# Performance work log

Measured on AMD Instinct MI355X. Metric: run time of the kernel, lower is better.

Reference implementation:

```python
import jax, jax.numpy as jnp
import numpy as np

N, E, D_IN, D, H = 50000, 600000, 128, 128, 128
NEG_SLOPE = 0.2  # PyG GATConv default


def setup_inputs() -> dict:
    key = jax.random.key(0)
    ks = jax.random.split(key, 10)
    s = 1.0 / np.sqrt(D)
    return {
        "x": jax.random.normal(ks[0], (N, D_IN), jnp.float32),
        "edge_index": jax.random.randint(ks[1], (2, E), 0, N, jnp.int64),
        "h": jax.random.normal(ks[2], (1, N, H), jnp.float32),
        "c": jax.random.normal(ks[3], (1, N, H), jnp.float32),
        "W": jax.random.normal(ks[4], (D_IN, D), jnp.float32) * s,
        "att_src": jax.random.normal(ks[5], (D,), jnp.float32) * s,
        "att_dst": jax.random.normal(ks[6], (D,), jnp.float32) * s,
        "bias_gat": jnp.zeros((D,), jnp.float32),
        "W_ih": jax.random.normal(ks[7], (4 * H, D), jnp.float32) * s,
        "W_hh": jax.random.normal(ks[8], (4 * H, H), jnp.float32) * s,
    }


def _gat_conv(x, edge_index, W, att_src, att_dst, bias_gat):
    n = x.shape[0]
    xs = x @ W  # [N, D]
    # add self loops (PyG default add_self_loops=True)
    loop = jnp.arange(n, dtype=edge_index.dtype)
    src = jnp.concatenate([edge_index[0], loop])
    dst = jnp.concatenate([edge_index[1], loop])
    a_src = xs @ att_src  # [N]
    a_dst = xs @ att_dst  # [N]
    e = a_src[src] + a_dst[dst]  # [E+N]
    e = jnp.where(e >= 0, e, NEG_SLOPE * e)  # leaky_relu
    # segment softmax over edges grouped by destination node
    e_max = jax.ops.segment_max(e, dst, num_segments=n)
    e_exp = jnp.exp(e - e_max[dst])
    e_sum = jax.ops.segment_sum(e_exp, dst, num_segments=n)
    alpha = e_exp / (e_sum[dst] + 1e-16)  # [E+N]
    out = jax.ops.segment_sum(alpha[:, None] * xs[src], dst, num_segments=n)
    return out + bias_gat


def _lstm_step(x, h0, c0, W_ih, W_hh):
    # torch LSTM gate order: i, f, g, o; bias=False
    gates = x @ W_ih.T + h0 @ W_hh.T  # [N, 4H]
    i, f, g, o = jnp.split(gates, 4, axis=-1)
    i, f, o = jax.nn.sigmoid(i), jax.nn.sigmoid(f), jax.nn.sigmoid(o)
    g = jnp.tanh(g)
    c1 = f * c0 + i * g
    h1 = o * jnp.tanh(c1)
    return h1, c1


def reference(x, edge_index, h, c, W, att_src, att_dst, bias_gat, W_ih, W_hh):
    xb = jnp.tanh(_gat_conv(x, edge_index, W, att_src, att_dst, bias_gat))  # [N, D]
    h1, c1 = _lstm_step(xb, h[0], c[0], W_ih, W_hh)
    # LSTM output for seq_len=1 equals the new hidden state
    return xb * 0 + h1, h1[None], c1[None]
```

## Files before the change

kernel.cpp:

```cpp
#include <hip/hip_runtime.h>
#include <hip/hip_bf16.h>
#include <math.h>

#define NEG 0.2f

typedef float f32x4 __attribute__((ext_vector_type(4)));
typedef short bf16x8 __attribute__((ext_vector_type(8)));

__device__ __forceinline__ float fsig(float x){ return 1.0f/(1.0f+__expf(-x)); }
__device__ __forceinline__ float ftanh(float x){ float e = __expf(2.0f*x); return 1.0f - 2.0f/(e+1.0f); }
__device__ __forceinline__ unsigned short f2bf(float v){
    __hip_bfloat16 b = __float2bfloat16(v);
    return *(unsigned short*)&b;
}
__device__ __forceinline__ bf16x8 pack8(float4 u, float4 v){
    bf16x8 r;
    r[0]=(short)f2bf(u.x); r[1]=(short)f2bf(u.y); r[2]=(short)f2bf(u.z); r[3]=(short)f2bf(u.w);
    r[4]=(short)f2bf(v.x); r[5]=(short)f2bf(v.y); r[6]=(short)f2bf(v.z); r[7]=(short)f2bf(v.w);
    return r;
}

__global__ void k_probe(const int* __restrict__ ei, int* __restrict__ flag){
    if(threadIdx.x==0){
        int nz=0;
        for(int i=0;i<64;i++) nz |= ei[2*i+1];
        *flag = (nz==0) ? 1 : 0;
    }
}

__global__ __launch_bounds__(256) void k_wpackx(const float* __restrict__ W,
                                                unsigned short* __restrict__ WPX){
    int f = blockIdx.x*256 + threadIdx.x;
    int l = f&63, ct = (f>>6)&7, ks = f>>9;
    int k0 = ks*32 + (l>>4)*8;
    int col = ct*16 + (l&15);
    #pragma unroll
    for(int j=0;j<8;j++) WPX[(size_t)f*8+j] = f2bf(W[(size_t)(k0+j)*128 + col]);
}

__global__ __launch_bounds__(256) void k_wtpack2(const float* __restrict__ W_ih,
                                                 const float* __restrict__ W_hh,
                                                 unsigned short* __restrict__ WP2){
    int f = blockIdx.x*256 + threadIdx.x;
    int l = f&63, ct = (f>>6)&3, ks = (f>>8)&7, g = f>>11;
    int k0 = ks*32 + (l>>4)*8;
    int col = ct*128 + g*16 + (l&15);
    #pragma unroll
    for(int j=0;j<8;j++){
        int k = k0+j;
        float w = (k<128) ? W_ih[(size_t)col*128+k] : W_hh[(size_t)col*128+(k-128)];
        WP2[(size_t)f*8+j] = f2bf(w);
    }
}

__global__ __launch_bounds__(256,2) void k_gemm_xs3(const float* __restrict__ x,
                                                    const unsigned short* __restrict__ WPX,
                                                    const float* __restrict__ att_s,
                                                    const float* __restrict__ att_d,
                                                    unsigned short* __restrict__ xsb,
                                                    float* __restrict__ a_src,
                                                    float* __restrict__ a_dst,
                                                    int n, int ntiles, int nwaves){
    const int w = threadIdx.x>>6, l = threadIdx.x&63;
    const int wid = blockIdx.x*4 + w;
    bf16x8 B[32];
    #pragma unroll
    for(int f=0;f<32;f++) B[f] = *(const bf16x8*)(WPX + (size_t)(f*64 + l)*8);
    float asv[8], adv[8];
    #pragma unroll
    for(int ct=0;ct<8;ct++){
        asv[ct] = att_s[ct*16 + (l&15)];
        adv[ct] = att_d[ct*16 + (l&15)];
    }
    for(int rt = wid; rt < ntiles; rt += nwaves){
        int arow = rt*16 + (l&15); if(arow>=n) arow = n-1;
        const float* xr = x + (size_t)arow*128 + (l>>4)*8;
        bf16x8 A[4];
        #pragma unroll
        for(int ks=0;ks<4;ks++){
            float4 u = *(const float4*)(xr + ks*32);
            float4 v = *(const float4*)(xr + ks*32 + 4);
            A[ks] = pack8(u,v);
        }
        f32x4 acc[8];
        #pragma unroll
        for(int ct=0;ct<8;ct++) acc[ct] = (f32x4){0.f,0.f,0.f,0.f};
        #pragma unroll
        for(int ks=0;ks<4;ks++){
            #pragma unroll
            for(int ct=0;ct<8;ct++)
                acc[ct] = __builtin_amdgcn_mfma_f32_16x16x32_bf16(A[ks], B[ks*8+ct], acc[ct], 0,0,0);
        }
        #pragma unroll
        for(int reg=0;reg<4;reg++){
            int row = rt*16 + (l>>4)*4 + reg;
            float ps=0.f, pd=0.f;
            #pragma unroll
            for(int ct=0;ct<8;ct++){ ps += acc[ct][reg]*asv[ct]; pd += acc[ct][reg]*adv[ct]; }
            ps += __shfl_xor(ps,1); pd += __shfl_xor(pd,1);
            ps += __shfl_xor(ps,2); pd += __shfl_xor(pd,2);
            ps += __shfl_xor(ps,4); pd += __shfl_xor(pd,4);
            ps += __shfl_xor(ps,8); pd += __shfl_xor(pd,8);
            if((l&15)==0 && row<n){ a_src[row]=ps; a_dst[row]=pd; }
            if(row<n){
                #pragma unroll
                for(int ct=0;ct<8;ct++)
                    xsb[(size_t)row*128 + ct*16 + (l&15)] = f2bf(acc[ct][reg]);
            }
        }
    }
}

__global__ __launch_bounds__(256) void k_hist(const int* __restrict__ ei,
                                              const int* __restrict__ flag,
                                              int* __restrict__ deg, int E, int EN){
    int e = blockIdx.x*256 + threadIdx.x;
    if(e>=EN) return;
    int dst = (e>=E) ? (e-E) : (*flag ? ei[2*(E+e)] : ei[E+e]);
    atomicAdd(&deg[dst], 1);
}

__global__ __launch_bounds__(256) void k_scan1(const int* __restrict__ deg,
                                               int* __restrict__ bsum, int n){
    __shared__ int ws[4];
    int b = blockIdx.x, t = threadIdx.x;
    int i = b*512 + t*2;
    int s = 0;
    if(i<n)   s += deg[i];
    if(i+1<n) s += deg[i+1];
    for(int off=32;off;off>>=1) s += __shfl_xor(s,off);
    if((t&63)==0) ws[t>>6]=s;
    __syncthreads();
    if(t==0) bsum[b]=ws[0]+ws[1]+ws[2]+ws[3];
}

__global__ void k_scan2(int* __restrict__ bsum, int* __restrict__ rowptr,
                        int nb, int n, int EN){
    int t = threadIdx.x;
    int v0 = (t<nb)    ? bsum[t]    : 0;
    int v1 = (64+t<nb) ? bsum[64+t] : 0;
    int x = v0;
    for(int d=1; d<64; d<<=1){ int y=__shfl_up(x,d); if(t>=d) x+=y; }
    int tot0 = __shfl(x,63);
    int x1 = v1;
    for(int d=1; d<64; d<<=1){ int y=__shfl_up(x1,d); if(t>=d) x1+=y; }
    if(t<nb)    bsum[t]    = x - v0;
    if(64+t<nb) bsum[64+t] = tot0 + x1 - v1;
    if(t==0) rowptr[n]=EN;
}

__global__ __launch_bounds__(256) void k_scan3(const int* __restrict__ deg,
                                               const int* __restrict__ bsum,
                                               int* __restrict__ rowptr,
                                               int* __restrict__ cursor, int n){
    __shared__ int wsum[4];
    int b = blockIdx.x, t = threadIdx.x;
    int i = b*512 + t*2;
    int d0 = (i<n)?deg[i]:0, d1 = (i+1<n)?deg[i+1]:0;
    int s = d0+d1;
    int x = s;
    int lane = t&63, wv = t>>6;
    for(int dd=1; dd<64; dd<<=1){ int y=__shfl_up(x,dd); if(lane>=dd) x+=y; }
    if(lane==63) wsum[wv]=x;
    __syncthreads();
    int woff=0;
    for(int w=0;w<wv;w++) woff += wsum[w];
    int ex = bsum[b] + woff + x - s;
    if(i<n)   { rowptr[i]  =ex;    cursor[i]  =ex;    }
    if(i+1<n) { rowptr[i+1]=ex+d0; cursor[i+1]=ex+d0; }
}

__global__ __launch_bounds__(256) void k_fill(const int* __restrict__ ei,
                                              const int* __restrict__ flag,
                                              int* __restrict__ cursor,
                                              int* __restrict__ csr_src, int E, int EN){
    int e = blockIdx.x*256 + threadIdx.x;
    if(e>=EN) return;
    int src,dst;
    if(e>=E){ src=dst=e-E; }
    else if(*flag){ src = ei[2*e]; dst = ei[2*(E+e)]; }
    else         { src = ei[e];   dst = ei[E+e]; }
    int pos = atomicAdd(&cursor[dst], 1);
    csr_src[pos] = src;
}

__global__ __launch_bounds__(256) void k_agg3(const int* __restrict__ rowptr,
                                              const int* __restrict__ csr_src,
                                              const float* __restrict__ a_src,
                                              const float* __restrict__ a_dst,
                                              const unsigned int* __restrict__ xsb32,
                                              const float* __restrict__ bg,
                                              const float* __restrict__ h0,
                                              unsigned short* __restrict__ xh, int n){
    const int wv = threadIdx.x>>6, l = threadIdx.x&63;
    const int dst = blockIdx.x*4 + wv;
    if(dst>=n) return;
    const int beg = rowptr[dst], end = rowptr[dst+1];
    const float ad = a_dst[dst];
    float ax=0.f, ay=0.f, psum=0.f;
    int j = beg;
    for(; j+8<=end; j+=8){
        int s0=csr_src[j],   s1=csr_src[j+1], s2=csr_src[j+2], s3=csr_src[j+3];
        int s4=csr_src[j+4], s5=csr_src[j+5], s6=csr_src[j+6], s7=csr_src[j+7];
        float e0=a_src[s0]+ad, e1=a_src[s1]+ad, e2=a_src[s2]+ad, e3=a_src[s3]+ad;
        float e4=a_src[s4]+ad, e5=a_src[s5]+ad, e6=a_src[s6]+ad, e7=a_src[s7]+ad;
        unsigned k0=xsb32[(size_t)s0*64+l], k1=xsb32[(size_t)s1*64+l];
        unsigned k2=xsb32[(size_t)s2*64+l], k3=xsb32[(size_t)s3*64+l];
        unsigned k4=xsb32[(size_t)s4*64+l], k5=xsb32[(size_t)s5*64+l];
        unsigned k6=xsb32[(size_t)s6*64+l], k7=xsb32[(size_t)s7*64+l];
        e0=e0>=0.f?e0:NEG*e0; e1=e1>=0.f?e1:NEG*e1; e2=e2>=0.f?e2:NEG*e2; e3=e3>=0.f?e3:NEG*e3;
        e4=e4>=0.f?e4:NEG*e4; e5=e5>=0.f?e5:NEG*e5; e6=e6>=0.f?e6:NEG*e6; e7=e7>=0.f?e7:NEG*e7;
        float p0=__expf(e0), p1=__expf(e1), p2=__expf(e2), p3=__expf(e3);
        float p4=__expf(e4), p5=__expf(e5), p6=__expf(e6), p7=__expf(e7);
        psum += (p0+p1+p2+p3)+(p4+p5+p6+p7);
        ax += p0*__uint_as_float(k0<<16) + p1*__uint_as_float(k1<<16)
            + p2*__uint_as_float(k2<<16) + p3*__uint_as_float(k3<<16)
            + p4*__uint_as_float(k4<<16) + p5*__uint_as_float(k5<<16)
            + p6*__uint_as_float(k6<<16) + p7*__uint_as_float(k7<<16);
        ay += p0*__uint_as_float(k0&0xffff0000u) + p1*__uint_as_float(k1&0xffff0000u)
            + p2*__uint_as_float(k2&0xffff0000u) + p3*__uint_as_float(k3&0xffff0000u)
            + p4*__uint_as_float(k4&0xffff0000u) + p5*__uint_as_float(k5&0xffff0000u)
            + p6*__uint_as_float(k6&0xffff0000u) + p7*__uint_as_float(k7&0xffff0000u);
    }
    for(; j<end; ++j){
        int s = csr_src[j];
        float sv = a_src[s]+ad;
        sv = sv>=0.f ? sv : NEG*sv;
        float p = __expf(sv);
        psum += p;
        unsigned pk = xsb32[(size_t)s*64 + l];
        ax += p*__uint_as_float(pk<<16);
        ay += p*__uint_as_float(pk & 0xffff0000u);
    }
    const float inv = 1.0f/(psum + 1e-16f);
    float t0 = ftanh(ax*inv + bg[2*l]);
    float t1 = ftanh(ay*inv + bg[2*l+1]);
    unsigned int pk = (unsigned)f2bf(t0) | ((unsigned)f2bf(t1)<<16);
    unsigned int* xr = (unsigned int*)(xh + (size_t)dst*256);
    xr[l] = pk;
    float2 hv = *(const float2*)(h0 + (size_t)dst*128 + 2*l);
    xr[64 + l] = (unsigned)f2bf(hv.x) | ((unsigned)f2bf(hv.y)<<16);
}

__global__ __launch_bounds__(256,4) void k_lstm9(const unsigned short* __restrict__ xh,
                                                 const unsigned short* __restrict__ WP2,
                                                 const float* __restrict__ c0,
                                                 float* __restrict__ out,
                                                 int n, int ntiles){
    __shared__ unsigned short Bl[16384];
    const int t = threadIdx.x;
    const int w = t>>6, l = t&63;
    const int rt = blockIdx.x*4 + w;
    const size_t nn = (size_t)n*128;
    const bool live = (rt < ntiles);
    bf16x8 A[8];
    if(live){
        int arow = rt*16 + (l&15); if(arow>=n) arow=n-1;
        const unsigned short* ar = xh + (size_t)arow*256 + (l>>4)*8;
        #pragma unroll
        for(int ks=0;ks<8;ks++) A[ks] = *(const bf16x8*)(ar + ks*32);
    }
    const int rbase = rt*16 + (l>>4)*4;
    for(int g=0; g<8; ++g){
        __syncthreads();
        {
            const float4* gsrc = (const float4*)(WP2 + (size_t)g*16384);
            float4* ldst = (float4*)Bl;
            #pragma unroll
            for(int i=0;i<8;i++) ldst[t + i*256] = gsrc[t + i*256];
        }
        __syncthreads();
        if(!live) continue;
        const int col = g*16 + (l&15);
        float cc[4];
        #pragma unroll
        for(int r=0;r<4;r++){ int rr=rbase+r; if(rr>=n) rr=n-1; cc[r]=c0[(size_t)rr*128+col]; }
        f32x4 acc[4];
        #pragma unroll
        for(int ct=0;ct<4;ct++) acc[ct] = (f32x4){0.f,0.f,0.f,0.f};
        #pragma unroll
        for(int ks=0;ks<8;ks++){
            #pragma unroll
            for(int ct=0;ct<4;ct++){
                const bf16x8 b = *(const bf16x8*)(Bl + ((ks*4+ct)*64 + l)*8);
                acc[ct] = __builtin_amdgcn_mfma_f32_16x16x32_bf16(A[ks], b, acc[ct], 0,0,0);
            }
        }
        #pragma unroll
        for(int reg=0;reg<4;reg++){
            int row = rbase + reg;
            if(row>=n) continue;
            float gi=acc[0][reg], gf=acc[1][reg], gg=acc[2][reg], go=acc[3][reg];
            float c1v = fsig(gf)*cc[reg] + fsig(gi)*ftanh(gg);
            float h1v = fsig(go)*ftanh(c1v);
            out[(size_t)row*128+col]        = h1v;
            out[nn + (size_t)row*128+col]   = h1v;
            out[2*nn + (size_t)row*128+col] = c1v;
        }
    }
}

extern "C" void kernel_launch(void* const* d_in, const int* in_sizes, int n_in,
                              void* d_out, int out_size, void* d_ws, size_t ws_size,
                              hipStream_t stream) {
    const float* x      = (const float*)d_in[0];
    const int*   ei     = (const int*)  d_in[1];
    const float* h      = (const float*)d_in[2];
    const float* c      = (const float*)d_in[3];
    const float* W      = (const float*)d_in[4];
    const float* atts   = (const float*)d_in[5];
    const float* attd   = (const float*)d_in[6];
    const float* bias   = (const float*)d_in[7];
    const float* W_ih   = (const float*)d_in[8];
    const float* W_hh   = (const float*)d_in[9];
    float* out = (float*)d_out;

    const int n  = in_sizes[0]/128;
    const int E  = in_sizes[1]/2;
    const int EN = E + n;
    const int NB = (n + 511)/512;
    const int ntiles = (n + 15)/16;
    const int n2 = ntiles*16;

    unsigned short* xsb = (unsigned short*)d_ws;
    unsigned short* xh  = xsb + (size_t)n*128;
    unsigned short* WP2 = xh + (size_t)n2*256;
    unsigned short* WPX = WP2 + 131072;
    float* a_src = (float*)(WPX + 16384);
    float* a_dst = a_src + n;
    int*   deg    = (int*)(a_dst + n);
    int*   rowptr = deg + n;
    int*   cursor = rowptr + n + 1;
    int*   bsum   = cursor + n;
    int*   csr_src= bsum + 128;
    int*   flag   = csr_src + EN;

    hipMemsetAsync(deg, 0, (size_t)n*sizeof(int), stream);
    k_probe<<<1,64,0,stream>>>(ei, flag);
    k_wpackx<<<8,256,0,stream>>>(W, WPX);
    k_wtpack2<<<64,256,0,stream>>>(W_ih, W_hh, WP2);
    k_gemm_xs3<<<1024,256,0,stream>>>(x, WPX, atts, attd, xsb, a_src, a_dst, n, ntiles, 4096);
    k_hist<<<(EN+255)/256,256,0,stream>>>(ei,flag,deg,E,EN);
    k_scan1<<<NB,256,0,stream>>>(deg,bsum,n);
    k_scan2<<<1,64,0,stream>>>(bsum,rowptr,NB,n,EN);
    k_scan3<<<NB,256,0,stream>>>(deg,bsum,rowptr,cursor,n);
    k_fill<<<(EN+255)/256,256,0,stream>>>(ei,flag,cursor,csr_src,E,EN);
    k_agg3<<<(n+3)/4,256,0,stream>>>(rowptr,csr_src,a_src,a_dst,(const unsigned int*)xsb,bias,h,xh,n);
    k_lstm9<<<(ntiles+3)/4,256,0,stream>>>(xh, WP2, c, out, n, ntiles);
}
```

Before: 173.8 us.

## Merge pack/probe/scan kernels and split LSTM gate groups across two blocks

Folds the two weight-pack kernels into one launch and removes the int64 probe kernel by doing a per-wave ballot check inside hist and fill. It also drops the scan2 kernel by having each scan3 block sum the preceding block totals itself. The LSTM kernel now launches twice as many blocks, each covering half the gate column groups with c0 preloaded, which raises parallelism but loads the A tiles twice. The aim is fewer launches and better LSTM occupancy, at the cost of redundant prefix and A-tile reads.

```diff
diff --git a/kernel.cpp b/kernel.cpp
--- a/kernel.cpp
+++ b/kernel.cpp
@@ -20,36 +20,30 @@
     return r;
 }
 
-__global__ void k_probe(const int* __restrict__ ei, int* __restrict__ flag){
-    if(threadIdx.x==0){
-        int nz=0;
-        for(int i=0;i<64;i++) nz |= ei[2*i+1];
-        *flag = (nz==0) ? 1 : 0;
-    }
-}
-
-__global__ __launch_bounds__(256) void k_wpackx(const float* __restrict__ W,
-                                                unsigned short* __restrict__ WPX){
-    int f = blockIdx.x*256 + threadIdx.x;
-    int l = f&63, ct = (f>>6)&7, ks = f>>9;
-    int k0 = ks*32 + (l>>4)*8;
-    int col = ct*16 + (l&15);
-    #pragma unroll
-    for(int j=0;j<8;j++) WPX[(size_t)f*8+j] = f2bf(W[(size_t)(k0+j)*128 + col]);
-}
-
-__global__ __launch_bounds__(256) void k_wtpack2(const float* __restrict__ W_ih,
-                                                 const float* __restrict__ W_hh,
-                                                 unsigned short* __restrict__ WP2){
-    int f = blockIdx.x*256 + threadIdx.x;
-    int l = f&63, ct = (f>>6)&3, ks = (f>>8)&7, g = f>>11;
-    int k0 = ks*32 + (l>>4)*8;
-    int col = ct*128 + g*16 + (l&15);
-    #pragma unroll
-    for(int j=0;j<8;j++){
-        int k = k0+j;
-        float w = (k<128) ? W_ih[(size_t)col*128+k] : W_hh[(size_t)col*128+(k-128)];
-        WP2[(size_t)f*8+j] = f2bf(w);
+__global__ __launch_bounds__(256) void k_pack(const float* __restrict__ W,
+                                              const float* __restrict__ W_ih,
+                                              const float* __restrict__ W_hh,
+                                              unsigned short* __restrict__ WPX,
+                                              unsigned short* __restrict__ WP2){
+    const int bid = blockIdx.x;
+    if(bid < 8){
+        int f = bid*256 + threadIdx.x;
+        int l = f&63, ct = (f>>6)&7, ks = f>>9;
+        int k0 = ks*32 + (l>>4)*8;
+        int col = ct*16 + (l&15);
+        #pragma unroll
+        for(int j=0;j<8;j++) WPX[(size_t)f*8+j] = f2bf(W[(size_t)(k0+j)*128 + col]);
+    } else {
+        int f = (bid-8)*256 + threadIdx.x;
+        int l = f&63, ct = (f>>6)&3, ks = (f>>8)&7, g = f>>11;
+        int k0 = ks*32 + (l>>4)*8;
+        int col = ct*128 + g*16 + (l&15);
+        #pragma unroll
+        for(int j=0;j<8;j++){
+            int k = k0+j;
+            float w = (k<128) ? W_ih[(size_t)col*128+k] : W_hh[(size_t)col*128+(k-128)];
+            WP2[(size_t)f*8+j] = f2bf(w);
+        }
     }
 }
 
@@ -112,11 +106,13 @@
 }
 
 __global__ __launch_bounds__(256) void k_hist(const int* __restrict__ ei,
-                                              const int* __restrict__ flag,
                                               int* __restrict__ deg, int E, int EN){
+    const int l = threadIdx.x & 63;
+    unsigned long long m = __ballot(ei[2*l+1] != 0);
+    const bool i64 = (m == 0ULL);
     int e = blockIdx.x*256 + threadIdx.x;
     if(e>=EN) return;
-    int dst = (e>=E) ? (e-E) : (*flag ? ei[2*(E+e)] : ei[E+e]);
+    int dst = (e>=E) ? (e-E) : (i64 ? ei[2*(size_t)(E+e)] : ei[(size_t)E+e]);
     atomicAdd(&deg[dst], 1);
 }
 
@@ -134,27 +130,20 @@
     if(t==0) bsum[b]=ws[0]+ws[1]+ws[2]+ws[3];
 }
 
-__global__ void k_scan2(int* __restrict__ bsum, int* __restrict__ rowptr,
-                        int nb, int n, int EN){
-    int t = threadIdx.x;
-    int v0 = (t<nb)    ? bsum[t]    : 0;
-    int v1 = (64+t<nb) ? bsum[64+t] : 0;
-    int x = v0;
-    for(int d=1; d<64; d<<=1){ int y=__shfl_up(x,d); if(t>=d) x+=y; }
-    int tot0 = __shfl(x,63);
-    int x1 = v1;
-    for(int d=1; d<64; d<<=1){ int y=__shfl_up(x1,d); if(t>=d) x1+=y; }
-    if(t<nb)    bsum[t]    = x - v0;
-    if(64+t<nb) bsum[64+t] = tot0 + x1 - v1;
-    if(t==0) rowptr[n]=EN;
-}
-
 __global__ __launch_bounds__(256) void k_scan3(const int* __restrict__ deg,
                                                const int* __restrict__ bsum,
                                                int* __restrict__ rowptr,
-                                               int* __restrict__ cursor, int n){
+                                               int* __restrict__ cursor,
+                                               int n, int EN){
     __shared__ int wsum[4];
+    __shared__ int boff;
     int b = blockIdx.x, t = threadIdx.x;
+    if(t < 64){
+        int a = 0;
+        for(int i=t; i<b; i+=64) a += bsum[i];
+        for(int off=32;off;off>>=1) a += __shfl_xor(a,off);
+        if(t==0) boff = a;
+    }
     int i = b*512 + t*2;
     int d0 = (i<n)?deg[i]:0, d1 = (i+1<n)?deg[i+1]:0;
     int s = d0+d1;
@@ -165,21 +154,24 @@
     __syncthreads();
     int woff=0;
     for(int w=0;w<wv;w++) woff += wsum[w];
-    int ex = bsum[b] + woff + x - s;
+    int ex = boff + woff + x - s;
     if(i<n)   { rowptr[i]  =ex;    cursor[i]  =ex;    }
     if(i+1<n) { rowptr[i+1]=ex+d0; cursor[i+1]=ex+d0; }
+    if(b==0 && t==0) rowptr[n]=EN;
 }
 
 __global__ __launch_bounds__(256) void k_fill(const int* __restrict__ ei,
-                                              const int* __restrict__ flag,
                                               int* __restrict__ cursor,
                                               int* __restrict__ csr_src, int E, int EN){
+    const int l = threadIdx.x & 63;
+    unsigned long long m = __ballot(ei[2*l+1] != 0);
+    const bool i64 = (m == 0ULL);
     int e = blockIdx.x*256 + threadIdx.x;
     if(e>=EN) return;
     int src,dst;
     if(e>=E){ src=dst=e-E; }
-    else if(*flag){ src = ei[2*e]; dst = ei[2*(E+e)]; }
-    else         { src = ei[e];   dst = ei[E+e]; }
+    else if(i64){ src = ei[2*(size_t)e]; dst = ei[2*(size_t)(E+e)]; }
+    else        { src = ei[(size_t)e];   dst = ei[(size_t)E+e]; }
     int pos = atomicAdd(&cursor[dst], 1);
     csr_src[pos] = src;
 }
@@ -242,17 +234,18 @@
     xr[64 + l] = (unsigned)f2bf(hv.x) | ((unsigned)f2bf(hv.y)<<16);
 }
 
-__global__ __launch_bounds__(256,4) void k_lstm9(const unsigned short* __restrict__ xh,
-                                                 const unsigned short* __restrict__ WP2,
-                                                 const float* __restrict__ c0,
-                                                 float* __restrict__ out,
-                                                 int n, int ntiles){
+__global__ __launch_bounds__(256,4) void k_lstm11(const unsigned short* __restrict__ xh,
+                                                  const unsigned short* __restrict__ WP2,
+                                                  const float* __restrict__ c0,
+                                                  float* __restrict__ out,
+                                                  int n, int ntiles){
     __shared__ unsigned short Bl[16384];
     const int t = threadIdx.x;
     const int w = t>>6, l = t&63;
-    const int rt = blockIdx.x*4 + w;
+    const int half = blockIdx.x & 1;
+    const int rt = (blockIdx.x>>1)*4 + w;
+    const bool live = (rt < ntiles);
     const size_t nn = (size_t)n*128;
-    const bool live = (rt < ntiles);
     bf16x8 A[8];
     if(live){
         int arow = rt*16 + (l&15); if(arow>=n) arow=n-1;
@@ -261,7 +254,18 @@
         for(int ks=0;ks<8;ks++) A[ks] = *(const bf16x8*)(ar + ks*32);
     }
     const int rbase = rt*16 + (l>>4)*4;
-    for(int g=0; g<8; ++g){
+    float cc[4][4];
+    if(live){
+        #pragma unroll
+        for(int gi=0;gi<4;gi++){
+            int col = (half*4+gi)*16 + (l&15);
+            #pragma unroll
+            for(int r=0;r<4;r++){ int rr=rbase+r; if(rr>=n) rr=n-1; cc[gi][r]=c0[(size_t)rr*128+col]; }
+        }
+    }
+    #pragma unroll
+    for(int gi=0; gi<4; ++gi){
+        const int g = half*4 + gi;
         __syncthreads();
         {
             const float4* gsrc = (const float4*)(WP2 + (size_t)g*16384);
@@ -272,9 +276,6 @@
         __syncthreads();
         if(!live) continue;
         const int col = g*16 + (l&15);
-        float cc[4];
-        #pragma unroll
-        for(int r=0;r<4;r++){ int rr=rbase+r; if(rr>=n) rr=n-1; cc[r]=c0[(size_t)rr*128+col]; }
         f32x4 acc[4];
         #pragma unroll
         for(int ct=0;ct<4;ct++) acc[ct] = (f32x4){0.f,0.f,0.f,0.f};
@@ -290,8 +291,8 @@
         for(int reg=0;reg<4;reg++){
             int row = rbase + reg;
             if(row>=n) continue;
-            float gi=acc[0][reg], gf=acc[1][reg], gg=acc[2][reg], go=acc[3][reg];
-            float c1v = fsig(gf)*cc[reg] + fsig(gi)*ftanh(gg);
+            float gi_=acc[0][reg], gf=acc[1][reg], gg=acc[2][reg], go=acc[3][reg];
+            float c1v = fsig(gf)*cc[gi][reg] + fsig(gi_)*ftanh(gg);
             float h1v = fsig(go)*ftanh(c1v);
             out[(size_t)row*128+col]        = h1v;
             out[nn + (size_t)row*128+col]   = h1v;
@@ -333,18 +334,14 @@
     int*   cursor = rowptr + n + 1;
     int*   bsum   = cursor + n;
     int*   csr_src= bsum + 128;
-    int*   flag   = csr_src + EN;
 
     hipMemsetAsync(deg, 0, (size_t)n*sizeof(int), stream);
-    k_probe<<<1,64,0,stream>>>(ei, flag);
-    k_wpackx<<<8,256,0,stream>>>(W, WPX);
-    k_wtpack2<<<64,256,0,stream>>>(W_ih, W_hh, WP2);
+    k_pack<<<72,256,0,stream>>>(W, W_ih, W_hh, WPX, WP2);
     k_gemm_xs3<<<1024,256,0,stream>>>(x, WPX, atts, attd, xsb, a_src, a_dst, n, ntiles, 4096);
-    k_hist<<<(EN+255)/256,256,0,stream>>>(ei,flag,deg,E,EN);
+    k_hist<<<(EN+255)/256,256,0,stream>>>(ei,deg,E,EN);
     k_scan1<<<NB,256,0,stream>>>(deg,bsum,n);
-    k_scan2<<<1,64,0,stream>>>(bsum,rowptr,NB,n,EN);
-    k_scan3<<<NB,256,0,stream>>>(deg,bsum,rowptr,cursor,n);
-    k_fill<<<(EN+255)/256,256,0,stream>>>(ei,flag,cursor,csr_src,E,EN);
+    k_scan3<<<NB,256,0,stream>>>(deg,bsum,rowptr,cursor,n,EN);
+    k_fill<<<(EN+255)/256,256,0,stream>>>(ei,cursor,csr_src,E,EN);
     k_agg3<<<(n+3)/4,256,0,stream>>>(rowptr,csr_src,a_src,a_dst,(const unsigned int*)xsb,bias,h,xh,n);
-    k_lstm9<<<(ntiles+3)/4,256,0,stream>>>(xh, WP2, c, out, n, ntiles);
-}
+    k_lstm11<<<2*((ntiles+3)/4),256,0,stream>>>(xh, WP2, c, out, n, ntiles);
+}
```

Result: faster. 168.1 us (-3.3%).
